# Optimization experiments

Hardware: AMD Instinct MI355X
Metric: run time of the kernel (lower is better)

Reference implementation:

```python
import jax, jax.numpy as jnp
import numpy as np

# ---- geometry constants (from init_kwargs options) ----
VIEWS, NDET, NX, NY = 360, 736, 512, 512
DVOX, DDET = 0.7, 1.2858
DSO, DOD = 595.0, 490.6
DSD = DSO + DOD
STEP = 0.0174533
END_ANGLE = STEP * VIEWS  # ~2*pi
EXTENT = 1


def _compute_indices():
    """CPU port of PixelIndexCal_cuda (fanflat mode, extent=1).
    Returns flat int64 indices of shape [NX*NY*VIEWS] (pixel-major, view inner)."""
    sVx, sVy = DVOX * NX, DVOX * NY
    alphas = np.linspace(0.0, END_ANGLE, VIEWS, endpoint=False)
    indX, indY = np.meshgrid(np.arange(NX, dtype=np.float64),
                             np.arange(NY, dtype=np.float64), indexing='ij')
    idx_all = np.empty((NX * NY, VIEWS), dtype=np.int64)
    for a in range(VIEWS):
        alpha = -alphas[a]
        c, s = np.cos(alpha), np.sin(alpha)
        P0x = -(sVx / 2 - DVOX / 2)
        P0y = sVy / 2 - DVOX / 2
        rot = lambda px, py: (px * c + py * s, -px * s + py * c)
        Px_, Py_ = rot(P0x, P0y)
        Pxx, Pxy = rot(P0x + DVOX, P0y)
        Pyx, Pyy = rot(P0x, P0y - DVOX)
        Py_, Pxy, Pyy = Py_ / DDET, Pxy / DDET, Pyy / DDET
        dXx, dXy = Pxx - Px_, Pxy - Py_
        dYx, dYy = Pyx - Px_, Pyy - Py_
        # per-pixel rotated coords
        Pix = Px_ + indX * dXx + indY * dYx
        Piy = Py_ + indX * dXy + indY * dYy
        # fanflat: source at (DSO, 0); ray hits detector plane at x = DSO-DSD
        vectX = Pix - DSO
        t = -DSD / vectX
        det = Piy * t + NDET / 2.0
        det = np.clip(det, 1.0, NDET - 2.0)
        idx_all[:, a] = (det + NDET * a).astype(np.int64).ravel()
    return idx_all.reshape(-1)


def _conv(x, w, b):
    y = jax.lax.conv_general_dilated(x, w, (1, 1), 'SAME',
                                     dimension_numbers=('NCHW', 'OIHW', 'NCHW'))
    return y + b[None, :, None, None]


def setup_inputs() -> dict:
    key = jax.random.key(0)
    ks = jax.random.split(key, 16)
    lin_std = 1.0 / np.sqrt(NDET)
    conv_std = 1.0 / np.sqrt(64 * 9)
    inp = {
        'x': jax.random.normal(ks[0], (1, 1, VIEWS, NDET), jnp.float32),
        'indices': jnp.asarray(_compute_indices()),
        'w1': jax.random.normal(ks[1], (NDET, NDET), jnp.float32) * lin_std,
        'b1': jnp.zeros((NDET,), jnp.float32),
        'w2': jax.random.normal(ks[2], (NDET, NDET), jnp.float32) * lin_std,
        'b2': jnp.zeros((NDET,), jnp.float32),
        'conv_in_w': jax.random.normal(ks[3], (64, 1, 3, 3), jnp.float32) * (1.0 / 3.0),
        'conv_in_b': jnp.zeros((64,), jnp.float32),
        'blk_w1': jax.random.normal(ks[4], (11, 64, 64, 3, 3), jnp.float32) * conv_std,
        'blk_b1': jnp.zeros((11, 64), jnp.float32),
        'blk_w2': jax.random.normal(ks[5], (11, 64, 64, 3, 3), jnp.float32) * conv_std,
        'blk_b2': jnp.zeros((11, 64), jnp.float32),
        'conv_out_w': jax.random.normal(ks[6], (1, 64, 3, 3), jnp.float32) * conv_std,
        'conv_out_b': jnp.zeros((1,), jnp.float32),
    }
    return inp


def reference(x, indices, w1, b1, w2, b2, conv_in_w, conv_in_b,
              blk_w1, blk_b1, blk_w2, blk_b2, conv_out_w, conv_out_b):
    # convf: two per-detector-row Linear+ReLU over last dim (nDetecU)
    h = jax.nn.relu(x @ w1.T + b1)
    h = jax.nn.relu(h @ w2.T + b2)
    # BackProjNet (learn=False): gather + sum over views, scale, flip
    sino = h.reshape(-1, 1, VIEWS * NDET)
    g = sino[:, :, indices]                         # [B,1,NX*NY*VIEWS]
    g = g.reshape(-1, 1, NX * NY, VIEWS * EXTENT)
    img = g.sum(axis=3) * ((END_ANGLE - 0.0) / (2 * VIEWS * EXTENT))
    img = img.reshape(-1, 1, NX, NY)
    img = jnp.flip(img, axis=(2, 3))
    # rCNN refinement: conv(1->64)+ReLU, 11 residual blocks, conv(64->1)
    y = jax.nn.relu(_conv(img, conv_in_w, conv_in_b))
    for i in range(11):
        z = _conv(y, blk_w1[i], blk_b1[i])
        z = jax.nn.relu(z)
        z = _conv(z, blk_w2[i], blk_b2[i])
        y = jax.nn.relu(y + z)
    out = _conv(y, conv_out_w, conv_out_b)
    return out
```

## Files before the change

### kernel.cpp

```cpp
#include <hip/hip_runtime.h>

#define VIEWS 360
#define NDET 736
#define NX 512
#define NY 512
#define NPIX (NX * NY)
#define ICP 72

typedef unsigned short u16;
typedef __attribute__((ext_vector_type(8))) short bf16x8;
typedef __attribute__((ext_vector_type(4))) float f32x4;

__device__ __forceinline__ u16 f2bf(float f) {
  unsigned u = __float_as_uint(f);
  return (u16)((u + 0x7fffu + ((u >> 16) & 1u)) >> 16);
}

__global__ __launch_bounds__(256) void linear_relu_kernel(
    const float* __restrict__ in, const float* __restrict__ w,
    const float* __restrict__ b, float* __restrict__ out) {
  __shared__ __align__(16) float xin[NDET];
  const int v = blockIdx.x;
  const float4* src4 = (const float4*)(in + v * NDET);
  float4* dst4 = (float4*)xin;
  for (int k = threadIdx.x; k < NDET / 4; k += 256) dst4[k] = src4[k];
  __syncthreads();

  for (int d = threadIdx.x; d < NDET; d += 256) {
    const float4* w4 = (const float4*)(w + d * NDET);
    float acc = 0.f;
#pragma unroll 8
    for (int k = 0; k < NDET / 4; ++k) {
      float4 xv = ((const float4*)xin)[k];
      float4 wv = w4[k];
      acc = fmaf(xv.x, wv.x, acc);
      acc = fmaf(xv.y, wv.y, acc);
      acc = fmaf(xv.z, wv.z, acc);
      acc = fmaf(xv.w, wv.w, acc);
    }
    out[v * NDET + d] = fmaxf(acc + b[d], 0.f);
  }
}

__global__ __launch_bounds__(256) void backproj_kernel(
    const float* __restrict__ sino, const int* __restrict__ idx,
    float* __restrict__ img) {
  const int p = blockIdx.x * 256 + threadIdx.x;
  const int4* ip4 = (const int4*)(idx + (size_t)p * VIEWS);
  float acc = 0.f;
#pragma unroll 5
  for (int a = 0; a < VIEWS / 4; ++a) {
    int4 v = ip4[a];
    acc += sino[v.x];
    acc += sino[v.y];
    acc += sino[v.z];
    acc += sino[v.w];
  }
  const int ix = p >> 9, iy = p & 511;
  const int q = (NX - 1 - ix) * NY + (NY - 1 - iy);
  img[q] = acc * 0.00872665f;
}

__device__ __forceinline__ void load9(const float* __restrict__ base, int gx,
                                      int gy, float v[9]) {
  const bool xm = gx > 0, xp = gx < NX - 1, ym = gy > 0, yp = gy < NY - 1;
  const float* c = base + gy * NX + gx;
  v[0] = (ym && xm) ? c[-NX - 1] : 0.f;
  v[1] = (ym)       ? c[-NX]     : 0.f;
  v[2] = (ym && xp) ? c[-NX + 1] : 0.f;
  v[3] = (xm)       ? c[-1]      : 0.f;
  v[4] =               c[0];
  v[5] = (xp)       ? c[1]       : 0.f;
  v[6] = (yp && xm) ? c[NX - 1]  : 0.f;
  v[7] = (yp)       ? c[NX]      : 0.f;
  v[8] = (yp && xp) ? c[NX + 1]  : 0.f;
}

__device__ __forceinline__ float dot9(float a, const float v[9],
                                      const float* __restrict__ w) {
  a = fmaf(v[0], w[0], a);
  a = fmaf(v[1], w[1], a);
  a = fmaf(v[2], w[2], a);
  a = fmaf(v[3], w[3], a);
  a = fmaf(v[4], w[4], a);
  a = fmaf(v[5], w[5], a);
  a = fmaf(v[6], w[6], a);
  a = fmaf(v[7], w[7], a);
  a = fmaf(v[8], w[8], a);
  return a;
}

__global__ __launch_bounds__(256) void conv_in_kernel(
    const float* __restrict__ in, const float* __restrict__ w,
    const float* __restrict__ b, float* __restrict__ out) {
  const int p = blockIdx.x * 256 + threadIdx.x;
  const int gx = p & (NX - 1), gy = p >> 9;
  float v[9];
  load9(in, gx, gy, v);
  float* o = out + (size_t)p * 64;
#pragma unroll
  for (int oc = 0; oc < 64; ++oc) {
    float a = dot9(b[oc], v, w + oc * 9);
    o[oc] = fmaxf(a, 0.f);
  }
}

__global__ __launch_bounds__(256) void prep_weights_kernel(
    const float* __restrict__ bw1, const float* __restrict__ bw2,
    u16* __restrict__ wAll) {
  const int g = blockIdx.x * 256 + threadIdx.x;
  if (g >= 22 * 36864) return;
  const int li = g / 36864, rm = g % 36864;
  const int oc = rm / 576, k = rm % 576;
  const int tap = k >> 6, ic = k & 63;
  const float* src = (li < 11) ? bw1 + li * 36864 : bw2 + (li - 11) * 36864;
  wAll[g] = f2bf(src[(oc * 64 + ic) * 9 + tap]);
}

template <int IN_BF, int OUT_BF, int RELU, int ADDRES>
__global__ __launch_bounds__(256, 2) void conv64_mfma(
    const void* __restrict__ in_, const u16* __restrict__ wA,
    const float* __restrict__ bias, const float* __restrict__ res,
    void* __restrict__ out_) {
  __shared__ u16 lds[6 * 66 * ICP];
  const int xb = (blockIdx.x & 7) * 64;
  const int yb = (int)(blockIdx.x >> 3) * 4;
  const int tid = threadIdx.x;

#pragma unroll 1
  for (int it = 0; it < 13; ++it) {
    const int g = it * 256 + tid;
    if (g < 3168) {
      const int icq = g & 7;
      const int xr = g >> 3;
      const int x66 = xr % 66;
      const int r = xr / 66;
      const int y = yb - 1 + r;
      const int x = xb - 1 + x66;
      uint4 d = {0u, 0u, 0u, 0u};
      if ((unsigned)y < 512u && (unsigned)x < 512u) {
        const size_t gi = ((size_t)((y << 9) + x)) * 64 + icq * 8;
        if (IN_BF) {
          d = *(const uint4*)&((const u16*)in_)[gi];
        } else {
          const float* s = &((const float*)in_)[gi];
          float4 f0 = *(const float4*)s;
          float4 f1 = *(const float4*)(s + 4);
          d.x = (unsigned)f2bf(f0.x) | ((unsigned)f2bf(f0.y) << 16);
          d.y = (unsigned)f2bf(f0.z) | ((unsigned)f2bf(f0.w) << 16);
          d.z = (unsigned)f2bf(f1.x) | ((unsigned)f2bf(f1.y) << 16);
          d.w = (unsigned)f2bf(f1.z) | ((unsigned)f2bf(f1.w) << 16);
        }
      }
      *(uint4*)&lds[xr * ICP + icq * 8] = d;
    }
  }
  __syncthreads();

  const int wv = tid >> 6;
  const int lane = tid & 63;
  const int n = lane & 15;
  const int kg = lane >> 4;

  f32x4 acc[4][4];
#pragma unroll
  for (int i = 0; i < 4; ++i)
#pragma unroll
    for (int j = 0; j < 4; ++j) acc[i][j] = (f32x4){0.f, 0.f, 0.f, 0.f};

#pragma unroll 1
  for (int tap = 0; tap < 9; ++tap) {
    const int r = wv + tap / 3;
    const int dxp1 = tap % 3;
#pragma unroll
    for (int kb = 0; kb < 2; ++kb) {
      const int icl = kb * 32 + kg * 8;
      const int k = tap * 64 + icl;
      bf16x8 afr[4];
#pragma unroll
      for (int mf = 0; mf < 4; ++mf)
        afr[mf] = *(const bf16x8*)&wA[(mf * 16 + n) * 576 + k];
      bf16x8 bfr[4];
#pragma unroll
      for (int nf = 0; nf < 4; ++nf)
        bfr[nf] = *(const bf16x8*)&lds[(r * 66 + dxp1 + nf * 16 + n) * ICP + icl];
#pragma unroll
      for (int mf = 0; mf < 4; ++mf)
#pragma unroll
        for (int nf = 0; nf < 4; ++nf)
          acc[mf][nf] = __builtin_amdgcn_mfma_f32_16x16x32_bf16(
              afr[mf], bfr[nf], acc[mf][nf], 0, 0, 0);
    }
  }

  const int y = yb + wv;
#pragma unroll
  for (int mf = 0; mf < 4; ++mf) {
    const float4 bv = *(const float4*)&bias[mf * 16 + kg * 4];
#pragma unroll
    for (int nf = 0; nf < 4; ++nf) {
      const int x = xb + nf * 16 + n;
      const size_t base = ((size_t)((y << 9) + x)) * 64 + mf * 16 + kg * 4;
      float v0 = acc[mf][nf][0] + bv.x;
      float v1 = acc[mf][nf][1] + bv.y;
      float v2 = acc[mf][nf][2] + bv.z;
      float v3 = acc[mf][nf][3] + bv.w;
      if (ADDRES) {
        float4 rr = *(const float4*)&res[base];
        v0 += rr.x; v1 += rr.y; v2 += rr.z; v3 += rr.w;
      }
      if (RELU) {
        v0 = fmaxf(v0, 0.f); v1 = fmaxf(v1, 0.f);
        v2 = fmaxf(v2, 0.f); v3 = fmaxf(v3, 0.f);
      }
      if (OUT_BF) {
        uint2 pk;
        pk.x = (unsigned)f2bf(v0) | ((unsigned)f2bf(v1) << 16);
        pk.y = (unsigned)f2bf(v2) | ((unsigned)f2bf(v3) << 16);
        *(uint2*)&((u16*)out_)[base] = pk;
      } else {
        *(float4*)&((float*)out_)[base] = (float4){v0, v1, v2, v3};
      }
    }
  }
}

__global__ __launch_bounds__(256) void conv_out_kernel(
    const float* __restrict__ in, const float* __restrict__ w,
    const float* __restrict__ b, float* __restrict__ out) {
  const int p = blockIdx.x * 256 + threadIdx.x;
  const int gx = p & (NX - 1), gy = p >> 9;
  float a = b[0];
#pragma unroll
  for (int ty = 0; ty < 3; ++ty) {
#pragma unroll
    for (int tx = 0; tx < 3; ++tx) {
      const int yy = gy + ty - 1, xx = gx + tx - 1;
      if ((unsigned)yy < 512u && (unsigned)xx < 512u) {
        const float* q = in + ((size_t)((yy << 9) + xx)) * 64;
        const int tap = ty * 3 + tx;
#pragma unroll 16
        for (int c = 0; c < 64; ++c) a = fmaf(q[c], w[c * 9 + tap], a);
      }
    }
  }
  out[p] = a;
}

extern "C" void kernel_launch(void* const* d_in, const int* in_sizes, int n_in,
                              void* d_out, int out_size, void* d_ws,
                              size_t ws_size, hipStream_t stream) {
  const float* x      = (const float*)d_in[0];
  const int*   indices= (const int*)d_in[1];
  const float* w1     = (const float*)d_in[2];
  const float* b1     = (const float*)d_in[3];
  const float* w2     = (const float*)d_in[4];
  const float* b2     = (const float*)d_in[5];
  const float* cin_w  = (const float*)d_in[6];
  const float* cin_b  = (const float*)d_in[7];
  const float* bw1    = (const float*)d_in[8];
  const float* bb1    = (const float*)d_in[9];
  const float* bw2    = (const float*)d_in[10];
  const float* bb2    = (const float*)d_in[11];
  const float* cout_w = (const float*)d_in[12];
  const float* cout_b = (const float*)d_in[13];

  float* ws   = (float*)d_ws;
  float* h1   = ws;
  float* h2   = h1 + VIEWS * NDET;
  float* img  = h2 + VIEWS * NDET;
  float* yf   = img + NPIX;
  u16*  zb    = (u16*)(yf + 64 * NPIX);
  u16*  wAll  = zb + 64 * NPIX;

  prep_weights_kernel<<<(22 * 36864 + 255) / 256, 256, 0, stream>>>(bw1, bw2,
                                                                    wAll);
  linear_relu_kernel<<<VIEWS, 256, 0, stream>>>(x, w1, b1, h1);
  linear_relu_kernel<<<VIEWS, 256, 0, stream>>>(h1, w2, b2, h2);
  backproj_kernel<<<NPIX / 256, 256, 0, stream>>>(h2, indices, img);
  conv_in_kernel<<<NPIX / 256, 256, 0, stream>>>(img, cin_w, cin_b, yf);

  for (int i = 0; i < 11; ++i) {
    conv64_mfma<0, 1, 1, 0><<<1024, 256, 0, stream>>>(
        yf, wAll + i * 36864, bb1 + i * 64, nullptr, zb);
    conv64_mfma<1, 0, 1, 1><<<1024, 256, 0, stream>>>(
        zb, wAll + (11 + i) * 36864, bb2 + i * 64, yf, yf);
  }
  conv_out_kernel<<<NPIX / 256, 256, 0, stream>>>(yf, cout_w, cout_b,
                                                  (float*)d_out);
}
```

Baseline: 2.231 ms.

## Swizzle conv LDS, prepack MFMA weights, coalesce backprojection and vectorize small convs

Backprojection now gives each pixel half a block, so threads read its indices contiguously, then sums them with a shared-memory tree reduction. This replaces the old per-thread strided index reads. The 64-channel MFMA conv drops padded LDS rows in favour of an XOR-swizzled layout, which shrinks LDS use and allows three blocks per CU. Weights are prepacked into per-lane fragment order and the next step's fragment is prefetched. conv_in and conv_out move to float4 stores and loads. The trade-off is many tiny blocks plus repeated syncs in backprojection, and more register pressure under the higher occupancy bound.

```diff
diff --git a/kernel.cpp b/kernel.cpp
--- a/kernel.cpp
+++ b/kernel.cpp
@@ -5,7 +5,6 @@
 #define NX 512
 #define NY 512
 #define NPIX (NX * NY)
-#define ICP 72
 
 typedef unsigned short u16;
 typedef __attribute__((ext_vector_type(8))) short bf16x8;
@@ -45,20 +44,26 @@
 __global__ __launch_bounds__(256) void backproj_kernel(
     const float* __restrict__ sino, const int* __restrict__ idx,
     float* __restrict__ img) {
-  const int p = blockIdx.x * 256 + threadIdx.x;
-  const int4* ip4 = (const int4*)(idx + (size_t)p * VIEWS);
-  float acc = 0.f;
-#pragma unroll 5
-  for (int a = 0; a < VIEWS / 4; ++a) {
-    int4 v = ip4[a];
-    acc += sino[v.x];
-    acc += sino[v.y];
-    acc += sino[v.z];
-    acc += sino[v.w];
-  }
-  const int ix = p >> 9, iy = p & 511;
-  const int q = (NX - 1 - ix) * NY + (NY - 1 - iy);
-  img[q] = acc * 0.00872665f;
+  __shared__ float red[256];
+  const int t = threadIdx.x;
+  const int half = t >> 7, j = t & 127;
+  const int p = blockIdx.x * 2 + half;
+  float part = 0.f;
+  if (j < 90) {
+    int4 v = *(const int4*)&idx[(size_t)p * VIEWS + j * 4];
+    part = sino[v.x] + sino[v.y] + sino[v.z] + sino[v.w];
+  }
+  red[t] = part;
+  __syncthreads();
+#pragma unroll
+  for (int s = 64; s > 0; s >>= 1) {
+    if ((t & 127) < s) red[t] += red[t + s];
+    __syncthreads();
+  }
+  if (j == 0) {
+    const int ix = p >> 9, iy = p & 511;
+    img[(NX - 1 - ix) * NY + (NY - 1 - iy)] = red[t] * 0.00872665f;
+  }
 }
 
 __device__ __forceinline__ void load9(const float* __restrict__ base, int gx,
@@ -97,32 +102,41 @@
   const int gx = p & (NX - 1), gy = p >> 9;
   float v[9];
   load9(in, gx, gy, v);
-  float* o = out + (size_t)p * 64;
-#pragma unroll
-  for (int oc = 0; oc < 64; ++oc) {
-    float a = dot9(b[oc], v, w + oc * 9);
-    o[oc] = fmaxf(a, 0.f);
+  float4* o = (float4*)(out + (size_t)p * 64);
+#pragma unroll
+  for (int oq = 0; oq < 16; ++oq) {
+    float4 r;
+    r.x = fmaxf(dot9(b[oq * 4 + 0], v, w + (oq * 4 + 0) * 9), 0.f);
+    r.y = fmaxf(dot9(b[oq * 4 + 1], v, w + (oq * 4 + 1) * 9), 0.f);
+    r.z = fmaxf(dot9(b[oq * 4 + 2], v, w + (oq * 4 + 2) * 9), 0.f);
+    r.w = fmaxf(dot9(b[oq * 4 + 3], v, w + (oq * 4 + 3) * 9), 0.f);
+    o[oq] = r;
   }
 }
 
 __global__ __launch_bounds__(256) void prep_weights_kernel(
     const float* __restrict__ bw1, const float* __restrict__ bw2,
-    u16* __restrict__ wAll) {
+    u16* __restrict__ wR) {
   const int g = blockIdx.x * 256 + threadIdx.x;
   if (g >= 22 * 36864) return;
-  const int li = g / 36864, rm = g % 36864;
-  const int oc = rm / 576, k = rm % 576;
-  const int tap = k >> 6, ic = k & 63;
+  const int li = g / 36864, r1 = g % 36864;
+  const int s = r1 / 2048, r2 = r1 % 2048;
+  const int lane = r2 / 32, r3 = r2 % 32;
+  const int mf = r3 / 8, j = r3 % 8;
+  const int tap = s >> 1, kb = s & 1;
+  const int kg = lane >> 4, n = lane & 15;
+  const int oc = mf * 16 + n;
+  const int ic = kb * 32 + kg * 8 + j;
   const float* src = (li < 11) ? bw1 + li * 36864 : bw2 + (li - 11) * 36864;
-  wAll[g] = f2bf(src[(oc * 64 + ic) * 9 + tap]);
+  wR[g] = f2bf(src[(oc * 64 + ic) * 9 + tap]);
 }
 
 template <int IN_BF, int OUT_BF, int RELU, int ADDRES>
-__global__ __launch_bounds__(256, 2) void conv64_mfma(
+__global__ __launch_bounds__(256, 3) void conv64_mfma(
     const void* __restrict__ in_, const u16* __restrict__ wA,
     const float* __restrict__ bias, const float* __restrict__ res,
     void* __restrict__ out_) {
-  __shared__ u16 lds[6 * 66 * ICP];
+  __shared__ u16 lds[6 * 66 * 64];
   const int xb = (blockIdx.x & 7) * 64;
   const int yb = (int)(blockIdx.x >> 3) * 4;
   const int tid = threadIdx.x;
@@ -152,7 +166,8 @@
           d.w = (unsigned)f2bf(f1.z) | ((unsigned)f2bf(f1.w) << 16);
         }
       }
-      *(uint4*)&lds[xr * ICP + icq * 8] = d;
+      const int slot = icq ^ (x66 & 7);
+      *(uint4*)&lds[(xr * 8 + slot) * 8] = d;
     }
   }
   __syncthreads();
@@ -168,29 +183,39 @@
 #pragma unroll
     for (int j = 0; j < 4; ++j) acc[i][j] = (f32x4){0.f, 0.f, 0.f, 0.f};
 
+  bf16x8 acur[4];
+#pragma unroll
+  for (int mf = 0; mf < 4; ++mf)
+    acur[mf] = *(const bf16x8*)&wA[(size_t)lane * 32 + mf * 8];
+
 #pragma unroll 1
-  for (int tap = 0; tap < 9; ++tap) {
+  for (int s = 0; s < 18; ++s) {
+    bf16x8 anxt[4];
+    const int sn = (s < 17) ? s + 1 : s;
+#pragma unroll
+    for (int mf = 0; mf < 4; ++mf)
+      anxt[mf] = *(const bf16x8*)&wA[((size_t)sn * 64 + lane) * 32 + mf * 8];
+
+    const int tap = s >> 1, kb = s & 1;
     const int r = wv + tap / 3;
     const int dxp1 = tap % 3;
-#pragma unroll
-    for (int kb = 0; kb < 2; ++kb) {
-      const int icl = kb * 32 + kg * 8;
-      const int k = tap * 64 + icl;
-      bf16x8 afr[4];
-#pragma unroll
-      for (int mf = 0; mf < 4; ++mf)
-        afr[mf] = *(const bf16x8*)&wA[(mf * 16 + n) * 576 + k];
-      bf16x8 bfr[4];
+    const int q = kb * 4 + kg;
+
+    bf16x8 bfr[4];
+#pragma unroll
+    for (int nf = 0; nf < 4; ++nf) {
+      const int xi = dxp1 + nf * 16 + n;
+      const int slot = q ^ (xi & 7);
+      bfr[nf] = *(const bf16x8*)&lds[((r * 66 + xi) * 8 + slot) * 8];
+    }
+#pragma unroll
+    for (int mf = 0; mf < 4; ++mf)
 #pragma unroll
       for (int nf = 0; nf < 4; ++nf)
-        bfr[nf] = *(const bf16x8*)&lds[(r * 66 + dxp1 + nf * 16 + n) * ICP + icl];
-#pragma unroll
-      for (int mf = 0; mf < 4; ++mf)
-#pragma unroll
-        for (int nf = 0; nf < 4; ++nf)
-          acc[mf][nf] = __builtin_amdgcn_mfma_f32_16x16x32_bf16(
-              afr[mf], bfr[nf], acc[mf][nf], 0, 0, 0);
-    }
+        acc[mf][nf] = __builtin_amdgcn_mfma_f32_16x16x32_bf16(
+            acur[mf], bfr[nf], acc[mf][nf], 0, 0, 0);
+#pragma unroll
+    for (int mf = 0; mf < 4; ++mf) acur[mf] = anxt[mf];
   }
 
   const int y = yb + wv;
@@ -237,10 +262,16 @@
     for (int tx = 0; tx < 3; ++tx) {
       const int yy = gy + ty - 1, xx = gx + tx - 1;
       if ((unsigned)yy < 512u && (unsigned)xx < 512u) {
-        const float* q = in + ((size_t)((yy << 9) + xx)) * 64;
+        const float4* q = (const float4*)(in + ((size_t)((yy << 9) + xx)) * 64);
         const int tap = ty * 3 + tx;
-#pragma unroll 16
-        for (int c = 0; c < 64; ++c) a = fmaf(q[c], w[c * 9 + tap], a);
+#pragma unroll
+        for (int i = 0; i < 16; ++i) {
+          float4 d = q[i];
+          a = fmaf(d.x, w[(i * 4 + 0) * 9 + tap], a);
+          a = fmaf(d.y, w[(i * 4 + 1) * 9 + tap], a);
+          a = fmaf(d.z, w[(i * 4 + 2) * 9 + tap], a);
+          a = fmaf(d.w, w[(i * 4 + 3) * 9 + tap], a);
+        }
       }
     }
   }
@@ -277,7 +308,7 @@
                                                                     wAll);
   linear_relu_kernel<<<VIEWS, 256, 0, stream>>>(x, w1, b1, h1);
   linear_relu_kernel<<<VIEWS, 256, 0, stream>>>(h1, w2, b2, h2);
-  backproj_kernel<<<NPIX / 256, 256, 0, stream>>>(h2, indices, img);
+  backproj_kernel<<<NPIX / 2, 256, 0, stream>>>(h2, indices, img);
   conv_in_kernel<<<NPIX / 256, 256, 0, stream>>>(img, cin_w, cin_b, yf);
 
   for (int i = 0; i < 11; ++i) {
```

Measured after the change: 2.183 ms. -2.1%, faster.
